# Optimization experiments

Hardware: AMD Instinct MI355X
Metric: run time of the kernel (lower is better)

The kernel has to match this reference:

```python
import jax, jax.numpy as jnp
import numpy as np

B, T, C = 4, 2048, 1024
H = 16
D = C // H  # head_dim = 64


def setup_inputs() -> dict:
    key = jax.random.key(0)
    ks = jax.random.split(key, 9)
    s = 1.0 / np.sqrt(C)
    return {
        "x": jax.random.normal(ks[0], (B, T, C), dtype=jnp.float32),
        "Wq": jax.random.normal(ks[1], (C, C), dtype=jnp.float32) * s,
        "bq": jnp.zeros((C,), dtype=jnp.float32),
        "Wk": jax.random.normal(ks[2], (C, C), dtype=jnp.float32) * s,
        "bk": jnp.zeros((C,), dtype=jnp.float32),
        "Wv": jax.random.normal(ks[3], (C, C), dtype=jnp.float32) * s,
        "bv": jnp.zeros((C,), dtype=jnp.float32),
        "Wp": jax.random.normal(ks[4], (C, C), dtype=jnp.float32) * s,
        "bp": jnp.zeros((C,), dtype=jnp.float32),
    }


def reference(x, Wq, bq, Wk, bk, Wv, bv, Wp, bp):
    # Linear projections; reshape to [B, H, T, D]
    def split_heads(y):
        return y.reshape(B, T, H, D).transpose(0, 2, 1, 3)

    q = split_heads(x @ Wq + bq)
    k = split_heads(x @ Wk + bk)
    v = split_heads(x @ Wv + bv)

    scale = 1.0 / np.sqrt(D)
    att = jnp.einsum('bhqd,bhkd->bhqk', q, k) * scale  # [B,H,T,T]
    att = jax.nn.softmax(att, axis=-1)
    # dropout with p=0.0 is identity
    out = jnp.einsum('bhqk,bhkd->bhqd', att, v)        # [B,H,T,D]
    out = out.transpose(0, 2, 1, 3).reshape(B, T, C)
    return out @ Wp + bp
```

## Files before the change

kernel.cpp:

```cpp
#include <hip/hip_runtime.h>


#define B_ 4
#define T_ 2048
#define C_ 1024
#define H_ 16
#define D_ 64

typedef float  f32x4  __attribute__((ext_vector_type(4)));
typedef __bf16 bf16x8 __attribute__((ext_vector_type(8)));
typedef __bf16 bf16x4 __attribute__((ext_vector_type(4)));

typedef const __attribute__((address_space(1))) void gv_t;
typedef __attribute__((address_space(3))) void lds_t;

__device__ __forceinline__ void async_load16(const void* g, void* l) {
  __builtin_amdgcn_global_load_lds((gv_t*)g, (lds_t*)l, 16, 0, 0);
}

__device__ __forceinline__ float fast_exp2(float x) {
#if __has_builtin(__builtin_amdgcn_exp2f)
  return __builtin_amdgcn_exp2f(x);
#else
  return exp2f(x);
#endif
}

__global__ __launch_bounds__(256) void cast_f32_bf16(
    const float* __restrict__ in, __bf16* __restrict__ out, int n) {
  int i = (blockIdx.x * 256 + threadIdx.x) * 8;
  if (i >= n) return;
  float4 a = *(const float4*)(in + i);
  float4 b = *(const float4*)(in + i + 4);
  bf16x8 o;
  o[0] = (__bf16)a.x; o[1] = (__bf16)a.y; o[2] = (__bf16)a.z; o[3] = (__bf16)a.w;
  o[4] = (__bf16)b.x; o[5] = (__bf16)b.y; o[6] = (__bf16)b.z; o[7] = (__bf16)b.w;
  *(bf16x8*)(out + i) = o;
}

__global__ __launch_bounds__(256) void transpose_cast_w(
    const float* __restrict__ W0, const float* __restrict__ W1,
    const float* __restrict__ W2, const float* __restrict__ W3,
    __bf16* __restrict__ out) {
  int z = blockIdx.z;
  const float* W = (z == 0) ? W0 : (z == 1) ? W1 : (z == 2) ? W2 : W3;
  __bf16* o = out + (size_t)z * (C_ * C_);
  __shared__ __align__(16) __bf16 sT[64][72];
  int tid = threadIdx.x;
  int n0 = blockIdx.x * 64, k0 = blockIdx.y * 64;
#pragma unroll
  for (int i = 0; i < 4; i++) {
    int s = tid + i * 256;
    int kr = s >> 4, nc = (s & 15) * 4;
    float4 v = *(const float4*)&W[(size_t)(k0 + kr) * C_ + n0 + nc];
    bf16x4 t;
    t[0] = (__bf16)v.x; t[1] = (__bf16)v.y; t[2] = (__bf16)v.z; t[3] = (__bf16)v.w;
    *(bf16x4*)&sT[kr][nc] = t;
  }
  __syncthreads();
#pragma unroll
  for (int i = 0; i < 2; i++) {
    int s = tid + i * 256;
    int nr = s >> 3, kc = (s & 7) * 8;
    bf16x8 ov;
#pragma unroll
    for (int j = 0; j < 8; j++) ov[j] = sT[kc + j][nr];
    *(bf16x8*)&o[(size_t)(n0 + nr) * C_ + k0 + kc] = ov;
  }
}

template <typename OutT, int EPI>
__device__ __forceinline__ void gemm_body(
    const __bf16* __restrict__ A, const __bf16* __restrict__ Bt,
    const float* __restrict__ bias, OutT* __restrict__ C, int M, int N, int K) {
  __shared__ __align__(16) __bf16 sA[128 * 32];
  __shared__ __align__(16) __bf16 sB[128 * 32];
  int tid = threadIdx.x, lane = tid & 63, wave = tid >> 6;
  int lr = lane & 15, quad = lane >> 4;
  int m0 = blockIdx.y * 128, n0 = blockIdx.x * 128;
  int wm = (wave & 1) * 64, wn = (wave >> 1) * 64;

  const f32x4 zero = {0.f, 0.f, 0.f, 0.f};
  f32x4 acc[4][4];
#pragma unroll
  for (int i = 0; i < 4; i++)
#pragma unroll
    for (int j = 0; j < 4; j++) acc[i][j] = zero;

  for (int k0 = 0; k0 < K; k0 += 32) {
    __syncthreads();
#pragma unroll
    for (int i = 0; i < 2; i++) {
      int s = tid + i * 256;
      int r = s >> 2, c8 = (s & 3) * 8;
      async_load16(A + (size_t)(m0 + r) * K + k0 + c8, &sA[s * 8]);
      async_load16(Bt + (size_t)(n0 + r) * K + k0 + c8, &sB[s * 8]);
    }
    __syncthreads();
    bf16x8 af[4], bfr[4];
#pragma unroll
    for (int mt = 0; mt < 4; mt++)
      af[mt] = *(const bf16x8*)&sA[(wm + mt * 16 + lr) * 32 + quad * 8];
#pragma unroll
    for (int nt = 0; nt < 4; nt++)
      bfr[nt] = *(const bf16x8*)&sB[(wn + nt * 16 + lr) * 32 + quad * 8];
#pragma unroll
    for (int mt = 0; mt < 4; mt++)
#pragma unroll
      for (int nt = 0; nt < 4; nt++)
        acc[mt][nt] = __builtin_amdgcn_mfma_f32_16x16x32_bf16(
            af[mt], bfr[nt], acc[mt][nt], 0, 0, 0);
  }
  if (EPI == 0) {
#pragma unroll
    for (int mt = 0; mt < 4; mt++) {
#pragma unroll
      for (int nt = 0; nt < 4; nt++) {
        int n = n0 + wn + nt * 16 + lr;
        float bv = bias[n];
#pragma unroll
        for (int r = 0; r < 4; r++) {
          int m = m0 + wm + mt * 16 + quad * 4 + r;
          C[(size_t)m * N + n] = (OutT)(acc[mt][nt][r] + bv);
        }
      }
    }
  } else {
    int bb = m0 >> 11;
    int mloc0 = (m0 & (T_ - 1)) + wm;
    __bf16* Ct = (__bf16*)C;
#pragma unroll
    for (int mt = 0; mt < 4; mt++) {
#pragma unroll
      for (int nt = 0; nt < 4; nt++) {
        int n = n0 + wn + nt * 16 + lr;
        float bv = bias[n];
        bf16x4 ov;
#pragma unroll
        for (int r = 0; r < 4; r++) ov[r] = (__bf16)(acc[mt][nt][r] + bv);
        *(bf16x4*)&Ct[((size_t)bb * C_ + n) * T_ + mloc0 + mt * 16 + quad * 4] = ov;
      }
    }
  }
}

__global__ __launch_bounds__(256) void gemm_qkv_kernel(
    const __bf16* __restrict__ A, const __bf16* __restrict__ WT,
    const float* __restrict__ b0, const float* __restrict__ b1,
    const float* __restrict__ b2, __bf16* __restrict__ qkbase,
    __bf16* __restrict__ Vt) {
  int z = blockIdx.z;
  if (z == 2) {
    gemm_body<__bf16, 1>(A, WT + (size_t)2 * C_ * C_, b2, Vt, B_ * T_, C_, C_);
  } else {
    const float* bias = (z == 0) ? b0 : b1;
    gemm_body<__bf16, 0>(A, WT + (size_t)z * C_ * C_, bias,
                         qkbase + (size_t)z * (B_ * T_) * C_, B_ * T_, C_, C_);
  }
}

__global__ __launch_bounds__(256) void gemm_proj_kernel(
    const __bf16* __restrict__ A, const __bf16* __restrict__ Bt,
    const float* __restrict__ bias, float* __restrict__ C) {
  gemm_body<float, 0>(A, Bt, bias, C, B_ * T_, C_, C_);
}

__global__ __launch_bounds__(256) void attn_kernel(
    const __bf16* __restrict__ Q, const __bf16* __restrict__ K,
    const __bf16* __restrict__ Vt, __bf16* __restrict__ O) {
  __shared__ __align__(16) __bf16 sK[64 * 72];
  __shared__ __align__(16) __bf16 sV[64 * 72];
  __shared__ __align__(16) __bf16 sP[4][32 * 72];
  int tid = threadIdx.x, wave = tid >> 6, lane = tid & 63;
  int lr = lane & 15, quad = lane >> 4;
  int bh = blockIdx.y;
  int b = bh >> 4, h = bh & 15;
  int qw = blockIdx.x * 128 + wave * 32;
  __bf16* sPw = &sP[wave][0];

  bf16x8 aq[2][2];
#pragma unroll
  for (int s = 0; s < 2; s++) {
    const __bf16* qp =
        Q + ((size_t)(b * T_ + qw + s * 16 + lr)) * C_ + h * D_ + quad * 8;
    aq[s][0] = *(const bf16x8*)qp;
    aq[s][1] = *(const bf16x8*)(qp + 32);
  }

  bf16x8 onesf;
#pragma unroll
  for (int j = 0; j < 8; j++) onesf[j] = (__bf16)1.0f;

  const f32x4 zero = {0.f, 0.f, 0.f, 0.f};
  f32x4 accO[2][4];
  f32x4 accL[2] = {zero, zero};
#pragma unroll
  for (int s = 0; s < 2; s++)
#pragma unroll
    for (int d = 0; d < 4; d++) accO[s][d] = zero;

  const float cexp = 0.125f * 1.44269504088896340736f;

  int srow[2], sc8[2];
#pragma unroll
  for (int i = 0; i < 2; i++) {
    int s = tid + i * 256;
    srow[i] = s >> 3;
    sc8[i] = (s & 7) * 8;
  }

  bf16x8 kreg[2], vreg[2];
#pragma unroll
  for (int i = 0; i < 2; i++) {
    kreg[i] = *(const bf16x8*)(K + ((size_t)(b * T_ + srow[i])) * C_ + h * D_ + sc8[i]);
    vreg[i] = *(const bf16x8*)(Vt + ((size_t)(bh * D_ + srow[i])) * T_ + sc8[i]);
  }

  for (int k0 = 0; k0 < T_; k0 += 64) {
    __syncthreads();
#pragma unroll
    for (int i = 0; i < 2; i++) {
      *(bf16x8*)&sK[srow[i] * 72 + sc8[i]] = kreg[i];
      *(bf16x8*)&sV[srow[i] * 72 + sc8[i]] = vreg[i];
    }
    __syncthreads();

    if (k0 + 64 < T_) {
      int kn = k0 + 64;
#pragma unroll
      for (int i = 0; i < 2; i++) {
        kreg[i] = *(const bf16x8*)(K + ((size_t)(b * T_ + kn + srow[i])) * C_ + h * D_ + sc8[i]);
        vreg[i] = *(const bf16x8*)(Vt + ((size_t)(bh * D_ + srow[i])) * T_ + kn + sc8[i]);
      }
    }

#pragma unroll
    for (int nt = 0; nt < 4; nt++) {
      bf16x8 bk0 = *(const bf16x8*)&sK[(nt * 16 + lr) * 72 + quad * 8];
      bf16x8 bk1 = *(const bf16x8*)&sK[(nt * 16 + lr) * 72 + 32 + quad * 8];
#pragma unroll
      for (int s = 0; s < 2; s++) {
        f32x4 z = zero;
        z = __builtin_amdgcn_mfma_f32_16x16x32_bf16(bk0, aq[s][0], z, 0, 0, 0);
        z = __builtin_amdgcn_mfma_f32_16x16x32_bf16(bk1, aq[s][1], z, 0, 0, 0);
        bf16x4 pk;
#pragma unroll
        for (int r = 0; r < 4; r++) pk[r] = (__bf16)fast_exp2(z[r] * cexp);
        *(bf16x4*)&sPw[(s * 16 + lr) * 72 + nt * 16 + quad * 4] = pk;
      }
    }

    bf16x8 bp[2][2];
#pragma unroll
    for (int s = 0; s < 2; s++) {
      bp[s][0] = *(const bf16x8*)&sPw[(s * 16 + lr) * 72 + quad * 8];
      bp[s][1] = *(const bf16x8*)&sPw[(s * 16 + lr) * 72 + 32 + quad * 8];
      accL[s] = __builtin_amdgcn_mfma_f32_16x16x32_bf16(onesf, bp[s][0], accL[s], 0, 0, 0);
      accL[s] = __builtin_amdgcn_mfma_f32_16x16x32_bf16(onesf, bp[s][1], accL[s], 0, 0, 0);
    }
#pragma unroll
    for (int dt = 0; dt < 4; dt++) {
      bf16x8 av0 = *(const bf16x8*)&sV[(dt * 16 + lr) * 72 + quad * 8];
      bf16x8 av1 = *(const bf16x8*)&sV[(dt * 16 + lr) * 72 + 32 + quad * 8];
#pragma unroll
      for (int s = 0; s < 2; s++) {
        accO[s][dt] = __builtin_amdgcn_mfma_f32_16x16x32_bf16(av0, bp[s][0], accO[s][dt], 0, 0, 0);
        accO[s][dt] = __builtin_amdgcn_mfma_f32_16x16x32_bf16(av1, bp[s][1], accO[s][dt], 0, 0, 0);
      }
    }
  }

#pragma unroll
  for (int s = 0; s < 2; s++) {
    float inv = 1.0f / accL[s][0];
    __bf16* op =
        O + ((size_t)(b * T_ + qw + s * 16 + lr)) * C_ + h * D_ + quad * 4;
#pragma unroll
    for (int dt = 0; dt < 4; dt++) {
      bf16x4 ov;
#pragma unroll
      for (int r = 0; r < 4; r++) ov[r] = (__bf16)(accO[s][dt][r] * inv);
      *(bf16x4*)&op[dt * 16] = ov;
    }
  }
}

extern "C" void kernel_launch(void* const* d_in, const int* in_sizes, int n_in,
                              void* d_out, int out_size, void* d_ws, size_t ws_size,
                              hipStream_t stream) {
  const float* x  = (const float*)d_in[0];
  const float* Wq = (const float*)d_in[1];
  const float* bq = (const float*)d_in[2];
  const float* Wk = (const float*)d_in[3];
  const float* bk = (const float*)d_in[4];
  const float* Wv = (const float*)d_in[5];
  const float* bv = (const float*)d_in[6];
  const float* Wp = (const float*)d_in[7];
  const float* bp = (const float*)d_in[8];
  float* out = (float*)d_out;

  char* ws = (char*)d_ws;
  const size_t MB = 1024 * 1024;
  __bf16* xb    = (__bf16*)(ws + 0 * MB);
  __bf16* WT    = (__bf16*)(ws + 16 * MB);
  __bf16* Qb    = (__bf16*)(ws + 24 * MB);
  __bf16* Kb    = Qb + (size_t)(B_ * T_) * C_;
  __bf16* Vt    = Kb + (size_t)(B_ * T_) * C_;
  __bf16* attnb = (__bf16*)(ws + 72 * MB);
  __bf16* WpT   = WT + (size_t)3 * C_ * C_;

  cast_f32_bf16<<<dim3(4096), dim3(256), 0, stream>>>(x, xb, B_ * T_ * C_);
  transpose_cast_w<<<dim3(16, 16, 4), dim3(256), 0, stream>>>(Wq, Wk, Wv, Wp, WT);
  gemm_qkv_kernel<<<dim3(8, 64, 3), dim3(256), 0, stream>>>(xb, WT, bq, bk, bv, Qb, Vt);
  attn_kernel<<<dim3(16, 64), dim3(256), 0, stream>>>(Qb, Kb, Vt, attnb);
  gemm_proj_kernel<<<dim3(8, 64), dim3(256), 0, stream>>>(attnb, WpT, bp, out);
}
```

Baseline: 300.5 us.

## Keep attention probabilities in registers via permlane16 swap and permuted V layout

Removes the per-wave LDS round trip for the softmax probability tile. Exponentiated scores are packed into registers and rearranged with v_permlane16_swap so they can feed the P·V MFMA directly. To match the resulting key ordering, the QKV GEMM epilogue writes V-transpose in a permuted column order. This saves LDS writes/reads and shared memory per block, but couples the attention kernel to a nonstandard Vt layout that must stay consistent.

```diff
diff --git a/kernel.cpp b/kernel.cpp
--- a/kernel.cpp
+++ b/kernel.cpp
@@ -10,6 +10,8 @@
 typedef float  f32x4  __attribute__((ext_vector_type(4)));
 typedef __bf16 bf16x8 __attribute__((ext_vector_type(8)));
 typedef __bf16 bf16x4 __attribute__((ext_vector_type(4)));
+typedef __bf16 bf16x2 __attribute__((ext_vector_type(2)));
+typedef unsigned uint2v __attribute__((ext_vector_type(2)));
 
 typedef const __attribute__((address_space(1))) void gv_t;
 typedef __attribute__((address_space(3))) void lds_t;
@@ -23,6 +25,16 @@
   return __builtin_amdgcn_exp2f(x);
 #else
   return exp2f(x);
+#endif
+}
+
+__device__ __forceinline__ void pl16_swap(unsigned& a, unsigned& b) {
+#if __has_builtin(__builtin_amdgcn_permlane16_swap)
+  uint2v r = __builtin_amdgcn_permlane16_swap(a, b, false, false);
+  a = r[0];
+  b = r[1];
+#else
+  asm("v_permlane16_swap_b32 %0, %1" : "+v"(a), "+v"(b));
 #endif
 }
 
@@ -131,6 +143,8 @@
     __bf16* Ct = (__bf16*)C;
 #pragma unroll
     for (int mt = 0; mt < 4; mt++) {
+      int pos = ((quad & 1) << 5) | ((((quad >> 1) << 1) | (mt & 1)) << 3) |
+                ((mt >> 1) << 2);
 #pragma unroll
       for (int nt = 0; nt < 4; nt++) {
         int n = n0 + wn + nt * 16 + lr;
@@ -138,7 +152,7 @@
         bf16x4 ov;
 #pragma unroll
         for (int r = 0; r < 4; r++) ov[r] = (__bf16)(acc[mt][nt][r] + bv);
-        *(bf16x4*)&Ct[((size_t)bb * C_ + n) * T_ + mloc0 + mt * 16 + quad * 4] = ov;
+        *(bf16x4*)&Ct[((size_t)bb * C_ + n) * T_ + mloc0 + pos] = ov;
       }
     }
   }
@@ -170,13 +184,11 @@
     const __bf16* __restrict__ Vt, __bf16* __restrict__ O) {
   __shared__ __align__(16) __bf16 sK[64 * 72];
   __shared__ __align__(16) __bf16 sV[64 * 72];
-  __shared__ __align__(16) __bf16 sP[4][32 * 72];
   int tid = threadIdx.x, wave = tid >> 6, lane = tid & 63;
   int lr = lane & 15, quad = lane >> 4;
   int bh = blockIdx.y;
   int b = bh >> 4, h = bh & 15;
   int qw = blockIdx.x * 128 + wave * 32;
-  __bf16* sPw = &sP[wave][0];
 
   bf16x8 aq[2][2];
 #pragma unroll
@@ -234,6 +246,7 @@
       }
     }
 
+    unsigned pw[2][4][2];
 #pragma unroll
     for (int nt = 0; nt < 4; nt++) {
       bf16x8 bk0 = *(const bf16x8*)&sK[(nt * 16 + lr) * 72 + quad * 8];
@@ -243,20 +256,30 @@
         f32x4 z = zero;
         z = __builtin_amdgcn_mfma_f32_16x16x32_bf16(bk0, aq[s][0], z, 0, 0, 0);
         z = __builtin_amdgcn_mfma_f32_16x16x32_bf16(bk1, aq[s][1], z, 0, 0, 0);
-        bf16x4 pk;
-#pragma unroll
-        for (int r = 0; r < 4; r++) pk[r] = (__bf16)fast_exp2(z[r] * cexp);
-        *(bf16x4*)&sPw[(s * 16 + lr) * 72 + nt * 16 + quad * 4] = pk;
-      }
-    }
-
-    bf16x8 bp[2][2];
+        union { bf16x2 h; unsigned u; } t0, t1;
+        t0.h[0] = (__bf16)fast_exp2(z[0] * cexp);
+        t0.h[1] = (__bf16)fast_exp2(z[1] * cexp);
+        t1.h[0] = (__bf16)fast_exp2(z[2] * cexp);
+        t1.h[1] = (__bf16)fast_exp2(z[3] * cexp);
+        pw[s][nt][0] = t0.u;
+        pw[s][nt][1] = t1.u;
+      }
+    }
+
+    bf16x8 bpA[2], bpB[2];
 #pragma unroll
     for (int s = 0; s < 2; s++) {
-      bp[s][0] = *(const bf16x8*)&sPw[(s * 16 + lr) * 72 + quad * 8];
-      bp[s][1] = *(const bf16x8*)&sPw[(s * 16 + lr) * 72 + 32 + quad * 8];
-      accL[s] = __builtin_amdgcn_mfma_f32_16x16x32_bf16(onesf, bp[s][0], accL[s], 0, 0, 0);
-      accL[s] = __builtin_amdgcn_mfma_f32_16x16x32_bf16(onesf, bp[s][1], accL[s], 0, 0, 0);
+      unsigned a0 = pw[s][0][0], b0 = pw[s][1][0]; pl16_swap(a0, b0);
+      unsigned a1 = pw[s][0][1], b1 = pw[s][1][1]; pl16_swap(a1, b1);
+      unsigned a2 = pw[s][2][0], b2 = pw[s][3][0]; pl16_swap(a2, b2);
+      unsigned a3 = pw[s][2][1], b3 = pw[s][3][1]; pl16_swap(a3, b3);
+      union { unsigned u[4]; bf16x8 v; } pA, pB;
+      pA.u[0] = a0; pA.u[1] = a1; pA.u[2] = a2; pA.u[3] = a3;
+      pB.u[0] = b0; pB.u[1] = b1; pB.u[2] = b2; pB.u[3] = b3;
+      bpA[s] = pA.v;
+      bpB[s] = pB.v;
+      accL[s] = __builtin_amdgcn_mfma_f32_16x16x32_bf16(onesf, bpA[s], accL[s], 0, 0, 0);
+      accL[s] = __builtin_amdgcn_mfma_f32_16x16x32_bf16(onesf, bpB[s], accL[s], 0, 0, 0);
     }
 #pragma unroll
     for (int dt = 0; dt < 4; dt++) {
@@ -264,8 +287,8 @@
       bf16x8 av1 = *(const bf16x8*)&sV[(dt * 16 + lr) * 72 + 32 + quad * 8];
 #pragma unroll
       for (int s = 0; s < 2; s++) {
-        accO[s][dt] = __builtin_amdgcn_mfma_f32_16x16x32_bf16(av0, bp[s][0], accO[s][dt], 0, 0, 0);
-        accO[s][dt] = __builtin_amdgcn_mfma_f32_16x16x32_bf16(av1, bp[s][1], accO[s][dt], 0, 0, 0);
+        accO[s][dt] = __builtin_amdgcn_mfma_f32_16x16x32_bf16(av0, bpA[s], accO[s][dt], 0, 0, 0);
+        accO[s][dt] = __builtin_amdgcn_mfma_f32_16x16x32_bf16(av1, bpB[s], accO[s][dt], 0, 0, 0);
       }
     }
   }
```

Result: faster. 291.1 us (-3.1%).
